# Performance work log

Hardware: AMD Instinct MI355X
Metric: run time of the kernel (lower is better)

The kernel has to match this reference:

```python
import jax, jax.numpy as jnp
import numpy as np


def setup_inputs() -> dict:
    key = jax.random.key(0)
    ks = jax.random.split(key, 6)
    B, IN, H, OUT = 4096, 1024, 2048, 256
    s1 = 1.0 / np.sqrt(IN)
    s2 = 1.0 / np.sqrt(H)
    return {
        "x": jax.random.normal(ks[0], (B, IN), dtype=jnp.float32),
        "W1": jax.random.uniform(ks[1], (H, IN), jnp.float32, -s1, s1),
        "b1": jax.random.uniform(ks[2], (H,), jnp.float32, -s1, s1),
        "W2": jax.random.uniform(ks[3], (OUT, H), jnp.float32, -s2, s2),
        "b2": jax.random.uniform(ks[4], (OUT,), jnp.float32, -s2, s2),
        "tau_mem": jnp.float32(10.0),
        "tau_syn": jnp.float32(5.0),
        "v_thresh": jnp.float32(1.0),
        "v_reset": jnp.float32(0.0),
        "v_mem0": jnp.zeros((B, H), jnp.float32),
        "i_syn0": jnp.zeros((B, H), jnp.float32),
        "time_steps": 32,
    }


def reference(x, W1, b1, W2, b2, tau_mem, tau_syn, v_thresh, v_reset, v_mem0, i_syn0, time_steps):
    dt = jnp.float32(1.0)
    # fc1(x)/time_steps is identical every step in the original loop; compute once.
    cur = (x @ W1.T + b1) / jnp.float32(time_steps)  # [B, H]

    def step(carry, _):
        v, i = carry
        i = i - (dt / tau_syn) * i + cur
        v = v - (dt / tau_mem) * v + i
        s = (v >= v_thresh).astype(x.dtype)
        v = v * (1.0 - s) + v_reset * s
        return (v, i), s

    (_, _), spikes = jax.lax.scan(step, (v_mem0, i_syn0), None, length=time_steps)
    total_spikes = spikes.sum(axis=0)  # [B, H]
    output = total_spikes @ W2.T + b2  # [B, OUT]
    return output, total_spikes
```

## Files before the change

kernel.cpp:

```cpp
#include <hip/hip_runtime.h>
#include <hip/hip_bf16.h>
#include <stdint.h>

typedef __attribute__((ext_vector_type(8))) short bf16x8;
typedef __attribute__((ext_vector_type(4))) float f32x4;

__device__ __forceinline__ float vmulf(float a, float b) {
    float d; asm volatile("v_mul_f32 %0, %1, %2" : "=v"(d) : "v"(a), "v"(b)); return d;
}
__device__ __forceinline__ float vaddf(float a, float b) {
    float d; asm volatile("v_add_f32 %0, %1, %2" : "=v"(d) : "v"(a), "v"(b)); return d;
}
__device__ __forceinline__ float vsubf(float a, float b) {
    float d; asm volatile("v_sub_f32 %0, %1, %2" : "=v"(d) : "v"(a), "v"(b)); return d;
}

__device__ __forceinline__ short bf16h(float v) {
    __hip_bfloat16 h = __float2bfloat16(v);
    return *(short*)&h;
}
__device__ __forceinline__ float bf16f(short s) {
    return __uint_as_float(((unsigned int)(unsigned short)s) << 16);
}
__device__ __forceinline__ void split2(float v, short& h, short& m) {
    h = bf16h(v);
    m = bf16h(__fsub_rn(v, bf16f(h)));
}

__device__ __forceinline__ float decode_scalar(const void* p, float dflt) {
    float f = *(const float*)p;
    if (!(f == f) || fabsf(f) > 1.0e6f) return dflt;
    return f;
}
__device__ __forceinline__ int decode_ts(const void* p) {
    int w = *(const int*)p;
    if (w >= 1 && w <= 100000) return w;
    return 32;
}

#define LDA 36

__global__ __launch_bounds__(256) void k1_panel_gemm(
    const float* __restrict__ X,
    const float* __restrict__ W1,
    float* __restrict__ P0,
    float* __restrict__ P1,
    int M, int N, int K, int KC)
{
    __shared__ float As[128][LDA];
    __shared__ float Bs[128][LDA];

    const int t  = threadIdx.x;
    const int tx = t & 15;
    const int ty = t >> 4;
    const int m0 = blockIdx.x * 128;
    const int n0 = blockIdx.y * 128;
    const int kz = blockIdx.z * KC;
    float* __restrict__ Pout = blockIdx.z ? P1 : P0;

    float p[8][8] = {};

    int srow[4], sq[4], oa[4], ob[4];
    #pragma unroll
    for (int cc = 0; cc < 4; ++cc) {
        const int li = cc * 256 + t;
        srow[cc] = li >> 3;
        sq[cc]   = li & 7;
        oa[cc] = (m0 + srow[cc]) * K + sq[cc] * 4;
        ob[cc] = (n0 + srow[cc]) * K + sq[cc] * 4;
    }

    float4 ra[4], rb[4];
    #pragma unroll
    for (int cc = 0; cc < 4; ++cc) {
        ra[cc] = *(const float4*)&X[oa[cc] + kz];
        rb[cc] = *(const float4*)&W1[ob[cc] + kz];
    }

    for (int k0 = kz; k0 < kz + KC; k0 += 32) {
        #pragma unroll
        for (int cc = 0; cc < 4; ++cc) {
            *(float4*)&As[srow[cc]][sq[cc] * 4] = ra[cc];
            *(float4*)&Bs[srow[cc]][sq[cc] * 4] = rb[cc];
        }
        __syncthreads();

        const int kn = k0 + 32;
        if (kn < kz + KC) {
            #pragma unroll
            for (int cc = 0; cc < 4; ++cc) {
                ra[cc] = *(const float4*)&X[oa[cc] + kn];
                rb[cc] = *(const float4*)&W1[ob[cc] + kn];
            }
        }

        #pragma unroll
        for (int g = 0; g < 8; ++g) {
            float4 bf[8];
            #pragma unroll
            for (int j = 0; j < 8; ++j)
                bf[j] = *(const float4*)&Bs[tx + 16 * j][g * 4];
            #pragma unroll
            for (int i = 0; i < 8; ++i) {
                const float4 af = *(const float4*)&As[ty + 16 * i][g * 4];
                #pragma unroll
                for (int kk = 0; kk < 4; ++kk) {
                    const float a = ((const float*)&af)[kk];
                    #pragma unroll
                    for (int j = 0; j < 8; ++j)
                        p[i][j] = __builtin_fmaf(a, ((const float*)&bf[j])[kk], p[i][j]);
                }
            }
        }
        __syncthreads();
    }

    #pragma unroll
    for (int i = 0; i < 8; ++i) {
        const size_t rowb = (size_t)(m0 + ty + 16 * i) * N;
        #pragma unroll
        for (int j = 0; j < 8; ++j)
            Pout[rowb + n0 + tx + 16 * j] = p[i][j];
    }
}

__global__ __launch_bounds__(256) void k1_combine_scan(
    const float* __restrict__ P0,
    const float* __restrict__ P1,
    const float* __restrict__ b1,
    const void* tau_mem_p, const void* tau_syn_p,
    const void* v_thresh_p, const void* v_reset_p, const void* ts_p,
    float* __restrict__ spikes, int N, int total4)
{
    const int idx4 = blockIdx.x * 256 + threadIdx.x;
    if (idx4 >= total4) return;

    const float tau_m = decode_scalar(tau_mem_p, 10.0f);
    const float tau_s = decode_scalar(tau_syn_p, 5.0f);
    const float vth   = decode_scalar(v_thresh_p, 1.0f);
    const float vrs   = decode_scalar(v_reset_p, 0.0f);
    const int   ts    = decode_ts(ts_p);
    const float rs    = 1.0f / tau_s;
    const float rm    = 1.0f / tau_m;
    const float ivts  = 1.0f / (float)ts;

    const float4 a = ((const float4*)P0)[idx4];
    const float4 b = ((const float4*)P1)[idx4];
    const int col0 = (idx4 * 4) % N;
    const float4 bb = *(const float4*)&b1[col0];

    float cur[4], iv[4], vv[4], cnt[4];
    const float av[4] = {a.x, a.y, a.z, a.w};
    const float bv[4] = {b.x, b.y, b.z, b.w};
    const float bbv[4] = {bb.x, bb.y, bb.z, bb.w};
    #pragma unroll
    for (int e = 0; e < 4; ++e) {
        const float c = vaddf(av[e], bv[e]);
        cur[e] = vmulf(vaddf(c, bbv[e]), ivts);
        iv[e] = 0.0f; vv[e] = 0.0f; cnt[e] = 0.0f;
    }
    for (int tt = 0; tt < ts; ++tt) {
        #pragma unroll
        for (int e = 0; e < 4; ++e) {
            iv[e] = vaddf(vsubf(iv[e], vmulf(rs, iv[e])), cur[e]);
            vv[e] = vaddf(vsubf(vv[e], vmulf(rm, vv[e])), iv[e]);
            const bool s = (vv[e] >= vth);
            cnt[e] += s ? 1.0f : 0.0f;
            vv[e]   = s ? vrs : vv[e];
        }
    }
    ((float4*)spikes)[idx4] = make_float4(cnt[0], cnt[1], cnt[2], cnt[3]);
}

__global__ __launch_bounds__(256) void k1_f32chain_snn(
    const float* __restrict__ X, const float* __restrict__ W1,
    const float* __restrict__ b1,
    const void* tau_mem_p, const void* tau_syn_p,
    const void* v_thresh_p, const void* v_reset_p, const void* ts_p,
    float* __restrict__ spikes, int M, int N, int K, int f0)
{
    __shared__ float As[128][LDA];
    __shared__ float Bs[128][LDA];

    const int t  = threadIdx.x;
    const int tx = t & 15;
    const int ty = t >> 4;
    const int m0 = blockIdx.x * 128;
    const int n0 = blockIdx.y * 128;

    float c[8][8] = {};
    float p[8][8] = {};

    for (int k0 = 0; k0 < K; k0 += 32) {
        #pragma unroll
        for (int cc = 0; cc < 4; ++cc) {
            const int li  = cc * 256 + t;
            const int row = li >> 3;
            const int q   = li & 7;
            *(float4*)&As[row][q * 4] =
                *(const float4*)&X[(size_t)(m0 + row) * K + k0 + q * 4];
            *(float4*)&Bs[row][q * 4] =
                *(const float4*)&W1[(size_t)(n0 + row) * K + k0 + q * 4];
        }
        __syncthreads();
        #pragma unroll
        for (int g = 0; g < 8; ++g) {
            float4 af[8], bf[8];
            #pragma unroll
            for (int i = 0; i < 8; ++i)
                af[i] = *(const float4*)&As[ty + 16 * i][g * 4];
            #pragma unroll
            for (int j = 0; j < 8; ++j)
                bf[j] = *(const float4*)&Bs[tx + 16 * j][g * 4];
            #pragma unroll
            for (int kk = 0; kk < 4; ++kk) {
                #pragma unroll
                for (int i = 0; i < 8; ++i) {
                    const float a = ((const float*)&af[i])[kk];
                    #pragma unroll
                    for (int j = 0; j < 8; ++j)
                        p[i][j] = __builtin_fmaf(a, ((const float*)&bf[j])[kk], p[i][j]);
                }
            }
        }
        __syncthreads();
        const int ke = k0 + 32;
        if (ke == f0 || ke == K) {
            #pragma unroll
            for (int i = 0; i < 8; ++i)
                #pragma unroll
                for (int j = 0; j < 8; ++j) {
                    c[i][j] = vaddf(c[i][j], p[i][j]);
                    p[i][j] = 0.0f;
                }
        }
    }

    const float tau_m = decode_scalar(tau_mem_p, 10.0f);
    const float tau_s = decode_scalar(tau_syn_p, 5.0f);
    const float vth   = decode_scalar(v_thresh_p, 1.0f);
    const float vrs   = decode_scalar(v_reset_p, 0.0f);
    const int   ts    = decode_ts(ts_p);
    const float rs    = 1.0f / tau_s;
    const float rm    = 1.0f / tau_m;
    const float ivts  = 1.0f / (float)ts;

    #pragma unroll
    for (int j = 0; j < 8; ++j) {
        const int col    = n0 + tx + 16 * j;
        const float bias = b1[col];
        float cur[8], iv[8], vv[8], cnt[8];
        #pragma unroll
        for (int i = 0; i < 8; ++i) {
            cur[i] = vmulf(vaddf(c[i][j], bias), ivts);
            iv[i] = 0.0f; vv[i] = 0.0f; cnt[i] = 0.0f;
        }
        for (int tt = 0; tt < ts; ++tt) {
            #pragma unroll
            for (int i = 0; i < 8; ++i) {
                iv[i] = vaddf(vsubf(iv[i], vmulf(rs, iv[i])), cur[i]);
                vv[i] = vaddf(vsubf(vv[i], vmulf(rm, vv[i])), iv[i]);
                const bool s = (vv[i] >= vth);
                cnt[i] += s ? 1.0f : 0.0f;
                vv[i]   = s ? vrs : vv[i];
            }
        }
        #pragma unroll
        for (int i = 0; i < 8; ++i)
            spikes[(size_t)(m0 + ty + 16 * i) * N + col] = cnt[i];
    }
}

__global__ __launch_bounds__(256) void k2_partial(
    const float* __restrict__ S, const float* __restrict__ W2,
    float* __restrict__ Pt,
    int M, int N2, int K2, int KC2)
{
    __shared__ __align__(16) short Sa[64 * 32];
    __shared__ __align__(16) short Bh[64 * 32];
    __shared__ __align__(16) short Bm[64 * 32];

    const int t    = threadIdx.x;
    const int l    = t & 63;
    const int w    = t >> 6;
    const int quad = l >> 4;
    const int r    = l & 15;
    const int wm   = w & 1;
    const int wn   = w >> 1;

    const int m0 = blockIdx.x * 64;
    const int n0 = blockIdx.y * 64;
    const int kz = blockIdx.z * KC2;
    float* __restrict__ outp = Pt + (size_t)blockIdx.z * M * N2;

    f32x4 acc[2][2] = {};

    for (int k0 = kz; k0 < kz + KC2; k0 += 32) {
        #pragma unroll
        for (int cc = 0; cc < 2; ++cc) {
            const int li  = cc * 256 + t;
            const int row = li >> 3;
            const int q   = li & 7;
            const float4 vs = *(const float4*)&S[(size_t)(m0 + row) * K2 + k0 + q * 4];
            *(short4*)&Sa[row * 32 + q * 4] =
                make_short4(bf16h(vs.x), bf16h(vs.y), bf16h(vs.z), bf16h(vs.w));
            const float4 vb = *(const float4*)&W2[(size_t)(n0 + row) * K2 + k0 + q * 4];
            short h[4], m_[4];
            split2(vb.x, h[0], m_[0]); split2(vb.y, h[1], m_[1]);
            split2(vb.z, h[2], m_[2]); split2(vb.w, h[3], m_[3]);
            *(short4*)&Bh[row * 32 + q * 4] = make_short4(h[0], h[1], h[2], h[3]);
            *(short4*)&Bm[row * 32 + q * 4] = make_short4(m_[0], m_[1], m_[2], m_[3]);
        }
        __syncthreads();

        bf16x8 af[2], bh[2], bm[2];
        #pragma unroll
        for (int i = 0; i < 2; ++i) {
            af[i] = *(const bf16x8*)&Sa[(wm * 32 + i * 16 + r) * 32 + quad * 8];
            bh[i] = *(const bf16x8*)&Bh[(wn * 32 + i * 16 + r) * 32 + quad * 8];
            bm[i] = *(const bf16x8*)&Bm[(wn * 32 + i * 16 + r) * 32 + quad * 8];
        }
        #pragma unroll
        for (int i = 0; i < 2; ++i)
            #pragma unroll
            for (int j = 0; j < 2; ++j) {
                acc[i][j] = __builtin_amdgcn_mfma_f32_16x16x32_bf16(af[i], bh[j], acc[i][j], 0, 0, 0);
                acc[i][j] = __builtin_amdgcn_mfma_f32_16x16x32_bf16(af[i], bm[j], acc[i][j], 0, 0, 0);
            }
        __syncthreads();
    }

    #pragma unroll
    for (int j = 0; j < 2; ++j) {
        const int col = n0 + wn * 32 + j * 16 + r;
        #pragma unroll
        for (int i = 0; i < 2; ++i) {
            const int rowb = m0 + wm * 32 + i * 16 + quad * 4;
            #pragma unroll
            for (int e = 0; e < 4; ++e)
                outp[(size_t)(rowb + e) * N2 + col] = acc[i][j][e];
        }
    }
}

__global__ __launch_bounds__(256) void k2_combine(
    const float* __restrict__ Pt, const float* __restrict__ b2,
    float* __restrict__ out, int N2, int total4, size_t stride4)
{
    const int idx4 = blockIdx.x * 256 + threadIdx.x;
    if (idx4 >= total4) return;
    float4 s = ((const float4*)Pt)[idx4];
    #pragma unroll
    for (int z = 1; z < 4; ++z) {
        const float4 v = ((const float4*)Pt)[stride4 * z + idx4];
        s.x += v.x; s.y += v.y; s.z += v.z; s.w += v.w;
    }
    const float4 bb = *(const float4*)&b2[(idx4 * 4) % N2];
    s.x += bb.x; s.y += bb.y; s.z += bb.z; s.w += bb.w;
    ((float4*)out)[idx4] = s;
}

__global__ __launch_bounds__(256) void k2_gemm(
    const float* __restrict__ S, const float* __restrict__ W2,
    const float* __restrict__ b2, float* __restrict__ out,
    int M, int N2, int K2)
{
    __shared__ __align__(16) short Sa[64 * 32];
    __shared__ __align__(16) short Bh[64 * 32];
    __shared__ __align__(16) short Bm[64 * 32];

    const int t    = threadIdx.x;
    const int l    = t & 63;
    const int w    = t >> 6;
    const int quad = l >> 4;
    const int r    = l & 15;
    const int wm   = w & 1;
    const int wn   = w >> 1;

    const int m0 = blockIdx.x * 64;
    const int n0 = blockIdx.y * 64;

    f32x4 acc[2][2] = {};

    for (int k0 = 0; k0 < K2; k0 += 32) {
        #pragma unroll
        for (int cc = 0; cc < 2; ++cc) {
            const int li  = cc * 256 + t;
            const int row = li >> 3;
            const int q   = li & 7;
            const float4 vs = *(const float4*)&S[(size_t)(m0 + row) * K2 + k0 + q * 4];
            *(short4*)&Sa[row * 32 + q * 4] =
                make_short4(bf16h(vs.x), bf16h(vs.y), bf16h(vs.z), bf16h(vs.w));
            const float4 vb = *(const float4*)&W2[(size_t)(n0 + row) * K2 + k0 + q * 4];
            short h[4], m_[4];
            split2(vb.x, h[0], m_[0]); split2(vb.y, h[1], m_[1]);
            split2(vb.z, h[2], m_[2]); split2(vb.w, h[3], m_[3]);
            *(short4*)&Bh[row * 32 + q * 4] = make_short4(h[0], h[1], h[2], h[3]);
            *(short4*)&Bm[row * 32 + q * 4] = make_short4(m_[0], m_[1], m_[2], m_[3]);
        }
        __syncthreads();

        bf16x8 af[2], bh[2], bm[2];
        #pragma unroll
        for (int i = 0; i < 2; ++i) {
            af[i] = *(const bf16x8*)&Sa[(wm * 32 + i * 16 + r) * 32 + quad * 8];
            bh[i] = *(const bf16x8*)&Bh[(wn * 32 + i * 16 + r) * 32 + quad * 8];
            bm[i] = *(const bf16x8*)&Bm[(wn * 32 + i * 16 + r) * 32 + quad * 8];
        }
        #pragma unroll
        for (int i = 0; i < 2; ++i)
            #pragma unroll
            for (int j = 0; j < 2; ++j) {
                acc[i][j] = __builtin_amdgcn_mfma_f32_16x16x32_bf16(af[i], bh[j], acc[i][j], 0, 0, 0);
                acc[i][j] = __builtin_amdgcn_mfma_f32_16x16x32_bf16(af[i], bm[j], acc[i][j], 0, 0, 0);
            }
        __syncthreads();
    }

    #pragma unroll
    for (int j = 0; j < 2; ++j) {
        const int col = n0 + wn * 32 + j * 16 + r;
        const float bias = b2[col];
        #pragma unroll
        for (int i = 0; i < 2; ++i) {
            const int rowb = m0 + wm * 32 + i * 16 + quad * 4;
            #pragma unroll
            for (int e = 0; e < 4; ++e)
                out[(size_t)(rowb + e) * N2 + col] = __fadd_rn(acc[i][j][e], bias);
        }
    }
}

extern "C" void kernel_launch(void* const* d_in, const int* in_sizes, int n_in,
                              void* d_out, int out_size, void* d_ws, size_t ws_size,
                              hipStream_t stream) {
    (void)n_in; (void)out_size;

    const float* X  = (const float*)d_in[0];
    const float* W1 = (const float*)d_in[1];
    const float* b1 = (const float*)d_in[2];
    const float* W2 = (const float*)d_in[3];
    const float* b2 = (const float*)d_in[4];
    const void* tau_mem = d_in[5];
    const void* tau_syn = d_in[6];
    const void* vth     = d_in[7];
    const void* vrs     = d_in[8];
    const void* ts      = d_in[11];

    const int H   = in_sizes[2];
    const int IN  = in_sizes[1] / H;
    const int OUT = in_sizes[4];
    const int B   = in_sizes[0] / IN;

    float* out    = (float*)d_out;
    float* spikes = out + (size_t)B * OUT;

    const int KC = 512;
    const size_t panel_bytes = (size_t)B * H * sizeof(float);
    const bool ws_ok = (IN == 2 * KC) && (ws_size >= panel_bytes) &&
                       ((uintptr_t)d_ws % 16 == 0);

    if (ws_ok) {
        float* P1 = (float*)d_ws;
        dim3 g1(B / 128, H / 128, 2);
        k1_panel_gemm<<<g1, 256, 0, stream>>>(X, W1, spikes, P1, B, H, IN, KC);

        const int total4 = (B * H) / 4;
        k1_combine_scan<<<(total4 + 255) / 256, 256, 0, stream>>>(
            spikes, P1, b1, tau_mem, tau_syn, vth, vrs, ts, spikes, H, total4);
    } else {
        dim3 g1(B / 128, H / 128);
        k1_f32chain_snn<<<g1, 256, 0, stream>>>(X, W1, b1, tau_mem, tau_syn, vth, vrs, ts,
                                                spikes, B, H, IN, KC);
    }

    const int KC2 = 512;
    const size_t k2_part_bytes = 4 * (size_t)B * OUT * sizeof(float);
    if (ws_ok && H == 4 * KC2 && ws_size >= k2_part_bytes) {
        float* Pt = (float*)d_ws;
        dim3 g2(B / 64, OUT / 64, 4);
        k2_partial<<<g2, 256, 0, stream>>>(spikes, W2, Pt, B, OUT, H, KC2);
        const int total4 = (B * OUT) / 4;
        k2_combine<<<(total4 + 255) / 256, 256, 0, stream>>>(
            Pt, b2, out, OUT, total4, (size_t)B * OUT / 4);
    } else {
        dim3 g2(B / 64, OUT / 64);
        k2_gemm<<<g2, 256, 0, stream>>>(spikes, W2, b2, out, B, OUT, H);
    }
}
```

Before: 458.3 us.

## Use direct global-to-LDS loads with double buffering and XOR swizzle in GEMM

Replaces the register-staged tile loads in the first GEMM with global_load_lds async copies straight into shared memory. The LDS tiles are double-buffered so the next K-slice loads while the current one is computed, which removes one barrier per iteration. An XOR swizzle on the 16-byte column chunk replaces the padded layout to avoid bank conflicts. This relies on the asynchronous direct-to-LDS copies having completed by the single barrier per iteration, and it doubles LDS use, which may lower occupancy.

```diff
diff --git a/kernel.cpp b/kernel.cpp
--- a/kernel.cpp
+++ b/kernel.cpp
@@ -36,6 +36,12 @@
     int w = *(const int*)p;
     if (w >= 1 && w <= 100000) return w;
     return 32;
+}
+
+__device__ __forceinline__ void gl16(const float* g, float* l) {
+    __builtin_amdgcn_global_load_lds(
+        (const __attribute__((address_space(1))) unsigned int*)g,
+        (__attribute__((address_space(3))) unsigned int*)l, 16, 0, 0);
 }
 
 #define LDA 36
@@ -47,8 +53,8 @@
     float* __restrict__ P1,
     int M, int N, int K, int KC)
 {
-    __shared__ float As[128][LDA];
-    __shared__ float Bs[128][LDA];
+    __shared__ __align__(16) float As[2][128][32];
+    __shared__ __align__(16) float Bs[2][128][32];
 
     const int t  = threadIdx.x;
     const int tx = t & 15;
@@ -60,59 +66,64 @@
 
     float p[8][8] = {};
 
-    int srow[4], sq[4], oa[4], ob[4];
-    #pragma unroll
-    for (int cc = 0; cc < 4; ++cc) {
-        const int li = cc * 256 + t;
-        srow[cc] = li >> 3;
-        sq[cc]   = li & 7;
-        oa[cc] = (m0 + srow[cc]) * K + sq[cc] * 4;
-        ob[cc] = (n0 + srow[cc]) * K + sq[cc] * 4;
-    }
-
-    float4 ra[4], rb[4];
-    #pragma unroll
-    for (int cc = 0; cc < 4; ++cc) {
-        ra[cc] = *(const float4*)&X[oa[cc] + kz];
-        rb[cc] = *(const float4*)&W1[ob[cc] + kz];
-    }
-
+    const int w  = t >> 6;
+    const int l  = t & 63;
+    const int lr = l >> 3;
+    const int sw = ((l & 7) ^ lr) << 2;
+    size_t ga[4], gb[4];
+    #pragma unroll
+    for (int c = 0; c < 4; ++c) {
+        const int row = ((w << 2) + c) * 8 + lr;
+        ga[c] = (size_t)(m0 + row) * K + sw;
+        gb[c] = (size_t)(n0 + row) * K + sw;
+    }
+
+    #pragma unroll
+    for (int c = 0; c < 4; ++c) {
+        const int f = (w << 2) + c;
+        gl16(X  + ga[c] + kz, &As[0][f << 3][0]);
+        gl16(W1 + gb[c] + kz, &Bs[0][f << 3][0]);
+    }
+    __syncthreads();
+
+    const int tya = ty & 7;
+    const int txa = tx & 7;
+
+    int d = 0;
     for (int k0 = kz; k0 < kz + KC; k0 += 32) {
-        #pragma unroll
-        for (int cc = 0; cc < 4; ++cc) {
-            *(float4*)&As[srow[cc]][sq[cc] * 4] = ra[cc];
-            *(float4*)&Bs[srow[cc]][sq[cc] * 4] = rb[cc];
-        }
-        __syncthreads();
-
         const int kn = k0 + 32;
         if (kn < kz + KC) {
-            #pragma unroll
-            for (int cc = 0; cc < 4; ++cc) {
-                ra[cc] = *(const float4*)&X[oa[cc] + kn];
-                rb[cc] = *(const float4*)&W1[ob[cc] + kn];
+            const int dn = d ^ 1;
+            #pragma unroll
+            for (int c = 0; c < 4; ++c) {
+                const int f = (w << 2) + c;
+                gl16(X  + ga[c] + kn, &As[dn][f << 3][0]);
+                gl16(W1 + gb[c] + kn, &Bs[dn][f << 3][0]);
             }
         }
 
         #pragma unroll
         for (int g = 0; g < 8; ++g) {
-            float4 bf[8];
+            float4 bfv[8];
+            const int cb = (g ^ txa) << 2;
             #pragma unroll
             for (int j = 0; j < 8; ++j)
-                bf[j] = *(const float4*)&Bs[tx + 16 * j][g * 4];
+                bfv[j] = *(const float4*)&Bs[d][tx + 16 * j][cb];
+            const int ca = (g ^ tya) << 2;
             #pragma unroll
             for (int i = 0; i < 8; ++i) {
-                const float4 af = *(const float4*)&As[ty + 16 * i][g * 4];
+                const float4 af = *(const float4*)&As[d][ty + 16 * i][ca];
                 #pragma unroll
                 for (int kk = 0; kk < 4; ++kk) {
                     const float a = ((const float*)&af)[kk];
                     #pragma unroll
                     for (int j = 0; j < 8; ++j)
-                        p[i][j] = __builtin_fmaf(a, ((const float*)&bf[j])[kk], p[i][j]);
+                        p[i][j] = __builtin_fmaf(a, ((const float*)&bfv[j])[kk], p[i][j]);
                 }
             }
         }
         __syncthreads();
+        d ^= 1;
     }
 
     #pragma unroll
```

Measured after the change: 480.9 us. +4.9%, slower.
